# Optimization experiments

Hardware: AMD Instinct MI355X
Metric: run time of the kernel (lower is better)

Reference implementation:

```python
import jax, jax.numpy as jnp
import numpy as np
from jax import lax


def _conv2d_same(x, w, b):
    # NHWC input, HWIO kernel, stride 1, SAME padding (matches keras Conv2D)
    y = lax.conv_general_dilated(x, w, window_strides=(1, 1), padding='SAME',
                                 dimension_numbers=('NHWC', 'HWIO', 'NHWC'))
    return y + b


def setup_inputs() -> dict:
    key = jax.random.key(0)
    k1, k2, k3, k4 = jax.random.split(key, 4)
    B, H, W, C = 16, 128, 128, 256
    F = 256
    inputs = jax.random.normal(k1, (B, H, W, C), dtype=jnp.float32)
    # offset conv: small random weights so offsets are non-trivial but in-range-ish
    w_off = jax.random.normal(k2, (3, 3, C, 2), dtype=jnp.float32) * 0.05
    b_off = jnp.zeros((2,), dtype=jnp.float32)
    w_def = jax.random.normal(k3, (3, 3, C, F), dtype=jnp.float32) * (1.0 / np.sqrt(9 * C))
    b_def = jax.random.normal(k4, (F,), dtype=jnp.float32) * 0.01
    return {"inputs": inputs, "w_off": w_off, "b_off": b_off,
            "w_def": w_def, "b_def": b_def}


def reference(inputs, w_off, b_off, w_def, b_def):
    B, H, W, C = inputs.shape
    # 1) predict per-pixel (dy, dx) offsets
    offsets = _conv2d_same(inputs, w_off, b_off)          # (B,H,W,2)
    off_h = offsets[..., 0]                               # (B,H,W)
    off_w = offsets[..., 1]                               # (B,H,W)
    # 2) build sampling grid, add offsets, clip, truncate to int (tf.cast semantics;
    #    values are non-negative after clip so truncation == floor)
    yy, xx = jnp.meshgrid(jnp.arange(H, dtype=inputs.dtype),
                          jnp.arange(W, dtype=inputs.dtype), indexing='ij')
    y = jnp.clip(yy[None] + off_h, 0.0, H - 1).astype(jnp.int32)   # (B,H,W)
    x = jnp.clip(xx[None] + off_w, 0.0, W - 1).astype(jnp.int32)   # (B,H,W)
    # 3) gather: one offset per pixel, shared across all channels
    lin = (y * W + x).reshape(B, H * W, 1)                # (B,HW,1)
    sampled = jnp.take_along_axis(inputs.reshape(B, H * W, C), lin, axis=1)
    sampled = sampled.reshape(B, H, W, C)
    # 4) main conv on resampled features
    return _conv2d_same(sampled, w_def, b_def)
```

## Files before the change

kernel.cpp:

```cpp
#include <hip/hip_runtime.h>
#include <hip/hip_bf16.h>

typedef __attribute__((ext_vector_type(8))) short bf16x8;
typedef __attribute__((ext_vector_type(4))) float f32x4;

__device__ __forceinline__ unsigned short f2bf(float f) {
  __hip_bfloat16 h = __float2bfloat16(f);
  return *reinterpret_cast<unsigned short*>(&h);
}

__device__ __forceinline__ void gld_lds16(void* lds, const void* g) {
  __builtin_amdgcn_global_load_lds(
      (const __attribute__((address_space(1))) unsigned int*)g,
      (__attribute__((address_space(3))) unsigned int*)lds, 16, 0, 0);
}

__global__ __launch_bounds__(256) void k1_offs_gather(
    const float* __restrict__ in, const float* __restrict__ w_off,
    const float* __restrict__ b_off, unsigned short* __restrict__ samp) {
  __shared__ float tile[6][128][20];
  __shared__ int lin_lds[512];

  const int bid = blockIdx.x;
  const int b = bid >> 5, h0 = (bid & 31) << 2;
  const int t = threadIdx.x;
  const int px_ = t & 127;
  const int rbase = t >> 7;

  double acY[2][4] = {{0, 0, 0, 0}, {0, 0, 0, 0}};
  double acX[2][4] = {{0, 0, 0, 0}, {0, 0, 0, 0}};

  for (int chunk = 0; chunk < 16; ++chunk) {
    const int c0 = chunk * 16;
    __syncthreads();
    #pragma unroll
    for (int it = 0; it < 12; ++it) {
      const int idx = it * 256 + t;
      const int row = idx >> 9;
      const int rest = idx & 511;
      const int px = rest >> 2, c4 = rest & 3;
      const int hh = h0 - 1 + row;
      float4 v = make_float4(0.f, 0.f, 0.f, 0.f);
      if ((unsigned)hh < 128u)
        v = *(const float4*)(in + ((size_t)(b * 128 + hh) * 128 + px) * 256 +
                             c0 + c4 * 4);
      *(float4*)&tile[row][px][c4 * 4] = v;
    }
    __syncthreads();
    #pragma unroll
    for (int tap = 0; tap < 9; ++tap) {
      const int dr = tap / 3, dc = tap % 3 - 1;
      const int wsrc = px_ + dc;
      if ((unsigned)wsrc >= 128u) continue;
      const float* wf = w_off + tap * 512 + chunk * 32;
      #pragma unroll
      for (int q = 0; q < 4; ++q) {
        const float4 v0 = *(const float4*)&tile[rbase + dr][wsrc][q * 4];
        const float4 v1 = *(const float4*)&tile[rbase + 2 + dr][wsrc][q * 4];
        const float* w8 = wf + q * 8;
        const double w0y = (double)w8[0], w0x = (double)w8[1];
        const double w1y = (double)w8[2], w1x = (double)w8[3];
        const double w2y = (double)w8[4], w2x = (double)w8[5];
        const double w3y = (double)w8[6], w3x = (double)w8[7];
        acY[0][q] += (double)v0.x * w0y; acX[0][q] += (double)v0.x * w0x;
        acY[0][q] += (double)v0.y * w1y; acX[0][q] += (double)v0.y * w1x;
        acY[0][q] += (double)v0.z * w2y; acX[0][q] += (double)v0.z * w2x;
        acY[0][q] += (double)v0.w * w3y; acX[0][q] += (double)v0.w * w3x;
        acY[1][q] += (double)v1.x * w0y; acX[1][q] += (double)v1.x * w0x;
        acY[1][q] += (double)v1.y * w1y; acX[1][q] += (double)v1.y * w1x;
        acY[1][q] += (double)v1.z * w2y; acX[1][q] += (double)v1.z * w2x;
        acY[1][q] += (double)v1.w * w3y; acX[1][q] += (double)v1.w * w3x;
      }
    }
  }
  {
    const double b0 = (double)b_off[0], b1 = (double)b_off[1];
    #pragma unroll
    for (int pi = 0; pi < 2; ++pi) {
      const int r = rbase + pi * 2;
      const int h = h0 + r;
      const double sy =
          (acY[pi][0] + acY[pi][1]) + (acY[pi][2] + acY[pi][3]);
      const double sx =
          (acX[pi][0] + acX[pi][1]) + (acX[pi][2] + acX[pi][3]);
      double yd = (double)h + (sy + b0);
      double xd = (double)px_ + (sx + b1);
      yd = yd < 0.0 ? 0.0 : (yd > 127.0 ? 127.0 : yd);
      xd = xd < 0.0 ? 0.0 : (xd > 127.0 ? 127.0 : xd);
      lin_lds[r * 128 + px_] = ((int)yd) * 128 + (int)xd;
    }
  }
  __syncthreads();
  const float* imgbase = in + (size_t)b * 16384 * 256;
  unsigned short* obase = samp + ((size_t)(b * 128 + h0)) * 128 * 256;
  #pragma unroll 4
  for (int it = 0; it < 128; ++it) {
    const int idx = it * 256 + t;
    const int p = idx >> 6, cv = idx & 63;
    const float4 v =
        *(const float4*)(imgbase + (size_t)lin_lds[p] * 256 + cv * 4);
    ushort4 o;
    o.x = f2bf(v.x); o.y = f2bf(v.y); o.z = f2bf(v.z); o.w = f2bf(v.w);
    *(ushort4*)(obase + (size_t)p * 256 + cv * 4) = o;
  }
}

__global__ __launch_bounds__(256) void k2_wT(const float* __restrict__ wdef,
                                             unsigned short* __restrict__ wT) {
  int g = blockIdx.x * 256 + threadIdx.x;
  int tap = g >> 16;
  int n = (g >> 8) & 255;
  int k = g & 255;
  wT[g] = f2bf(wdef[((size_t)tap * 256 + k) * 256 + n]);
}

struct Frags { bf16x8 a[8]; bf16x8 b[4]; };

__global__ __launch_bounds__(512, 2) void k3_conv(
    const unsigned short* __restrict__ samp, const unsigned short* __restrict__ wT,
    const float* __restrict__ b_def, float* __restrict__ out,
    const unsigned short* __restrict__ zerobuf) {
  __shared__ __align__(16) unsigned char smem[131072];

  const int bid0 = blockIdx.x;
  const int mt = (bid0 & 7) * 128 + (bid0 >> 3);
  const int bimg = mt >> 6;
  const int h0 = (mt & 63) * 2;

  const int tid = threadIdx.x;
  const int lane = tid & 63, wave = tid >> 6;
  const int wr = wave >> 2, wc = wave & 3;
  const int r15 = lane & 15, g4 = lane >> 4;
  const int g4eff = g4 ^ ((r15 >> 1) & 3);

  const char* sA = (const char*)smem + (wr * 128 + r15) * 64 + g4eff * 16;
  const char* sB = (const char*)smem + 65536 + (wc * 64 + r15) * 64 + g4eff * 16;

  const int chq = tid & 3;
  const int pix = tid >> 2;
  const int chs = chq ^ ((pix >> 1) & 3);
  const unsigned short* pA[2];
  const unsigned short* pB[2];
  unsigned vmask[2];
  #pragma unroll
  for (int it = 0; it < 2; ++it) {
    const int hh = h0 + it;
    pA[it] = samp + ((size_t)(bimg * 128 + hh) * 128 + pix) * 256 + chs * 8;
    pB[it] = wT + (size_t)(it * 128 + pix) * 256 + chs * 8;
    unsigned m = 0;
    #pragma unroll
    for (int tap = 0; tap < 9; ++tap) {
      const int dr = tap / 3 - 1, dc = tap % 3 - 1;
      if ((unsigned)(hh + dr) < 128u && (unsigned)(pix + dc) < 128u)
        m |= 1u << tap;
    }
    vmask[it] = m;
  }
  const unsigned short* zb = zerobuf + chq * 8;

  f32x4 acc[8][4];
  #pragma unroll
  for (int i = 0; i < 8; ++i)
    #pragma unroll
    for (int j = 0; j < 4; ++j) acc[i][j] = (f32x4){0.f, 0.f, 0.f, 0.f};

  auto stage = [&](int ts, int SLOT) {
    const int tap = ts >> 3, kc = ts & 7;
    const int q = (tap * 11) >> 5;
    const int tapdelta = ((q - 1) * 128 + (tap - q * 3 - 1)) * 256 + kc * 32;
    const int boffg = tap * 65536 + kc * 32;
    unsigned char* Ad = smem + SLOT * 16384;
    unsigned char* Bd = smem + 65536 + SLOT * 16384;
    #pragma unroll
    for (int it = 0; it < 2; ++it)
      gld_lds16(Bd + (it * 512 + tid) * 16, pB[it] + boffg);
    #pragma unroll
    for (int it = 0; it < 2; ++it) {
      const unsigned short* src =
          ((vmask[it] >> tap) & 1) ? (pA[it] + tapdelta) : zb;
      gld_lds16(Ad + (it * 512 + tid) * 16, src);
    }
  };

  auto readfr = [&](Frags& f, int SLOT) {
    #pragma unroll
    for (int ni = 0; ni < 4; ++ni)
      f.b[ni] = *(const bf16x8*)(sB + SLOT * 16384 + ni * 1024);
    #pragma unroll
    for (int mi = 0; mi < 8; ++mi)
      f.a[mi] = *(const bf16x8*)(sA + SLOT * 16384 + mi * 1024);
  };

  auto launder = [&](Frags& f) {
    #pragma unroll
    for (int i = 0; i < 8; ++i) asm volatile("" : "+v"(f.a[i]));
    #pragma unroll
    for (int i = 0; i < 4; ++i) asm volatile("" : "+v"(f.b[i]));
  };

  auto mfma32 = [&](Frags& f) {
    #pragma unroll
    for (int mi = 0; mi < 8; ++mi)
      #pragma unroll
      for (int ni = 0; ni < 4; ++ni)
        acc[mi][ni] = __builtin_amdgcn_mfma_f32_16x16x32_bf16(
            f.a[mi], f.b[ni], acc[mi][ni], 0, 0, 0);
  };

  Frags fr0, fr1;

#define K3_STEP(T_RT, SLOT_NXT, FR_CUR, FR_NXT, DO_READS, DO_STAGE, VMSTR) \
  {                                                                        \
    asm volatile("s_waitcnt lgkmcnt(0)" ::: "memory");                     \
    launder(FR_CUR);                                                       \
    __builtin_amdgcn_sched_barrier(0);                                     \
    __builtin_amdgcn_s_setprio(1);                                         \
    if (DO_READS) readfr(FR_NXT, SLOT_NXT);                                \
    if (DO_STAGE) stage((T_RT) + 3, ((SLOT_NXT) + 2) & 3);                 \
    mfma32(FR_CUR);                                                        \
    if (DO_READS && DO_STAGE) {                                            \
      _Pragma("unroll")                                                    \
      for (int u = 0; u < 4; ++u) {                                        \
        __builtin_amdgcn_sched_group_barrier(0x008, 8, 0);                 \
        __builtin_amdgcn_sched_group_barrier(0x100, 3, 0);                 \
        __builtin_amdgcn_sched_group_barrier(0x030, 1, 0);                 \
      }                                                                    \
    }                                                                      \
    __builtin_amdgcn_s_setprio(0);                                         \
    __builtin_amdgcn_sched_barrier(0);                                     \
    asm volatile("s_waitcnt " VMSTR ::: "memory");                         \
    __builtin_amdgcn_s_barrier();                                          \
    asm volatile("" ::: "memory");                                         \
  }

  stage(0, 0); stage(1, 1); stage(2, 2);
  asm volatile("s_waitcnt vmcnt(4)" ::: "memory");
  __builtin_amdgcn_s_barrier();
  asm volatile("" ::: "memory");
  readfr(fr0, 0);

  for (int tb = 0; tb < 68; tb += 4) {
    K3_STEP(tb + 0, 1, fr0, fr1, true, true, "vmcnt(4)");
    K3_STEP(tb + 1, 2, fr1, fr0, true, true, "vmcnt(4)");
    K3_STEP(tb + 2, 3, fr0, fr1, true, true, "vmcnt(4)");
    K3_STEP(tb + 3, 0, fr1, fr0, true, true, "vmcnt(4)");
  }
  K3_STEP(68, 1, fr0, fr1, true, true,  "vmcnt(4)");
  K3_STEP(69, 2, fr1, fr0, true, false, "vmcnt(0)");
  K3_STEP(70, 3, fr0, fr1, true, false, "vmcnt(0)");
  {
    asm volatile("s_waitcnt lgkmcnt(0)" ::: "memory");
    launder(fr1);
    __builtin_amdgcn_sched_barrier(0);
    mfma32(fr1);
  }
#undef K3_STEP

  const int colg = wc * 64 + r15;
  float bias[4];
  #pragma unroll
  for (int ni = 0; ni < 4; ++ni) bias[ni] = b_def[colg + ni * 16];
  #pragma unroll
  for (int mi = 0; mi < 8; ++mi) {
    const int r0 = wr * 128 + mi * 16 + g4 * 4;
    #pragma unroll
    for (int j = 0; j < 4; ++j) {
      float* orow = out + ((size_t)mt * 256 + r0 + j) * 256 + colg;
      #pragma unroll
      for (int ni = 0; ni < 4; ++ni) orow[ni * 16] = acc[mi][ni][j] + bias[ni];
    }
  }
}

extern "C" void kernel_launch(void* const* d_in, const int* in_sizes, int n_in,
                              void* d_out, int out_size, void* d_ws, size_t ws_size,
                              hipStream_t stream) {
  const float* in = (const float*)d_in[0];
  const float* w_off = (const float*)d_in[1];
  const float* b_off = (const float*)d_in[2];
  const float* w_def = (const float*)d_in[3];
  const float* b_def = (const float*)d_in[4];
  float* out = (float*)d_out;

  char* ws = (char*)d_ws;
  unsigned short* zerobuf = (unsigned short*)ws;
  unsigned short* wT = (unsigned short*)(ws + 4096);
  unsigned short* samp = (unsigned short*)(ws + 4096 + 1179648);

  hipMemsetAsync(ws, 0, 4096, stream);
  hipLaunchKernelGGL(k2_wT, dim3(2304), dim3(256), 0, stream, w_def, wT);
  hipLaunchKernelGGL(k1_offs_gather, dim3(512), dim3(256), 0, stream,
                     in, w_off, b_off, samp);
  hipLaunchKernelGGL(k3_conv, dim3(1024), dim3(512), 0, stream,
                     samp, wT, b_def, out, zerobuf);
}
```

Before: 585.6 us.

## Enlarge offset-conv tile to 8 rows, stage offset weights in LDS

The offset-conv plus gather kernel now has each block cover 8 output rows with 512 threads instead of 4 rows with 256. This cuts the halo-row reloads from 50% to 25% extra. The channel chunk is halved to 8 so the 10-row input tile still fits in LDS. The per-chunk offset weights are staged into LDS rather than read from global memory inside the tap loop. The trade-offs are twice as many chunk iterations and barriers, only 256 blocks on the device, and fewer double-precision accumulators per thread.

Result: faster. 523.3 us (-10.6%).

```diff
diff --git a/kernel.cpp b/kernel.cpp
--- a/kernel.cpp
+++ b/kernel.cpp
@@ -15,36 +15,40 @@
       (__attribute__((address_space(3))) unsigned int*)lds, 16, 0, 0);
 }
 
-__global__ __launch_bounds__(256) void k1_offs_gather(
+__global__ __launch_bounds__(512) void k1_offs_gather(
     const float* __restrict__ in, const float* __restrict__ w_off,
     const float* __restrict__ b_off, unsigned short* __restrict__ samp) {
-  __shared__ float tile[6][128][20];
-  __shared__ int lin_lds[512];
+  __shared__ float tile[10][128][12];
+  __shared__ float wlf[144];
+  __shared__ int lin_lds[1024];
 
   const int bid = blockIdx.x;
-  const int b = bid >> 5, h0 = (bid & 31) << 2;
+  const int b = bid >> 4, h0 = (bid & 15) << 3;
   const int t = threadIdx.x;
   const int px_ = t & 127;
-  const int rbase = t >> 7;
-
-  double acY[2][4] = {{0, 0, 0, 0}, {0, 0, 0, 0}};
-  double acX[2][4] = {{0, 0, 0, 0}, {0, 0, 0, 0}};
-
-  for (int chunk = 0; chunk < 16; ++chunk) {
-    const int c0 = chunk * 16;
+  const int rb = t >> 7;
+
+  double acY[2][2] = {{0, 0}, {0, 0}};
+  double acX[2][2] = {{0, 0}, {0, 0}};
+
+  for (int chunk = 0; chunk < 32; ++chunk) {
+    const int c0 = chunk * 8;
     __syncthreads();
-    #pragma unroll
-    for (int it = 0; it < 12; ++it) {
-      const int idx = it * 256 + t;
-      const int row = idx >> 9;
-      const int rest = idx & 511;
-      const int px = rest >> 2, c4 = rest & 3;
+    if (t < 144) {
+      const int tap = t >> 4, r = t & 15;
+      wlf[t] = w_off[tap * 512 + (c0 + (r >> 1)) * 2 + (r & 1)];
+    }
+    #pragma unroll
+    for (int it = 0; it < 5; ++it) {
+      const int idx = it * 512 + t;
+      const int row = idx >> 8;
+      const int px = (idx & 255) >> 1, q = idx & 1;
       const int hh = h0 - 1 + row;
       float4 v = make_float4(0.f, 0.f, 0.f, 0.f);
       if ((unsigned)hh < 128u)
         v = *(const float4*)(in + ((size_t)(b * 128 + hh) * 128 + px) * 256 +
-                             c0 + c4 * 4);
-      *(float4*)&tile[row][px][c4 * 4] = v;
+                             c0 + q * 4);
+      *(float4*)&tile[row][px][q * 4] = v;
     }
     __syncthreads();
     #pragma unroll
@@ -52,11 +56,11 @@
       const int dr = tap / 3, dc = tap % 3 - 1;
       const int wsrc = px_ + dc;
       if ((unsigned)wsrc >= 128u) continue;
-      const float* wf = w_off + tap * 512 + chunk * 32;
+      const float* wf = &wlf[tap * 16];
       #pragma unroll
-      for (int q = 0; q < 4; ++q) {
-        const float4 v0 = *(const float4*)&tile[rbase + dr][wsrc][q * 4];
-        const float4 v1 = *(const float4*)&tile[rbase + 2 + dr][wsrc][q * 4];
+      for (int q = 0; q < 2; ++q) {
+        const float4 v0 = *(const float4*)&tile[rb + dr][wsrc][q * 4];
+        const float4 v1 = *(const float4*)&tile[rb + 4 + dr][wsrc][q * 4];
         const float* w8 = wf + q * 8;
         const double w0y = (double)w8[0], w0x = (double)w8[1];
         const double w1y = (double)w8[2], w1x = (double)w8[3];
@@ -77,12 +81,10 @@
     const double b0 = (double)b_off[0], b1 = (double)b_off[1];
     #pragma unroll
     for (int pi = 0; pi < 2; ++pi) {
-      const int r = rbase + pi * 2;
+      const int r = rb + pi * 4;
       const int h = h0 + r;
-      const double sy =
-          (acY[pi][0] + acY[pi][1]) + (acY[pi][2] + acY[pi][3]);
-      const double sx =
-          (acX[pi][0] + acX[pi][1]) + (acX[pi][2] + acX[pi][3]);
+      const double sy = acY[pi][0] + acY[pi][1];
+      const double sx = acX[pi][0] + acX[pi][1];
       double yd = (double)h + (sy + b0);
       double xd = (double)px_ + (sx + b1);
       yd = yd < 0.0 ? 0.0 : (yd > 127.0 ? 127.0 : yd);
@@ -95,7 +97,7 @@
   unsigned short* obase = samp + ((size_t)(b * 128 + h0)) * 128 * 256;
   #pragma unroll 4
   for (int it = 0; it < 128; ++it) {
-    const int idx = it * 256 + t;
+    const int idx = it * 512 + t;
     const int p = idx >> 6, cv = idx & 63;
     const float4 v =
         *(const float4*)(imgbase + (size_t)lin_lds[p] * 256 + cv * 4);
@@ -289,7 +291,7 @@
 
   hipMemsetAsync(ws, 0, 4096, stream);
   hipLaunchKernelGGL(k2_wT, dim3(2304), dim3(256), 0, stream, w_def, wT);
-  hipLaunchKernelGGL(k1_offs_gather, dim3(512), dim3(256), 0, stream,
+  hipLaunchKernelGGL(k1_offs_gather, dim3(256), dim3(512), 0, stream,
                      in, w_off, b_off, samp);
   hipLaunchKernelGGL(k3_conv, dim3(1024), dim3(512), 0, stream,
                      samp, wT, b_def, out, zerobuf);
```
